# Optimization experiments

Hardware: AMD Instinct MI355X
Metric: run time of the kernel (lower is better)

## Reference

```python
import jax, jax.numpy as jnp
import numpy as np

B, C, K = 8192, 4096, 4096
BK, BN = 1, 16          # block-sparse tile sizes (bk x bn)
KEEP = 0.3


def setup_inputs() -> dict:
    key = jax.random.key(0)
    kx, kw, kb, km = jax.random.split(key, 4)
    stdv = 1.0 / np.sqrt(C * K)  # reset_parameters uses 1/sqrt(C*K)
    x = jax.random.normal(kx, (B, C), dtype=jnp.float32)
    weight = jax.random.uniform(kw, (K, C), dtype=jnp.float32, minval=-stdv, maxval=stdv)
    # block mask on (K/bk, C/bn) grid, expanded to full weight shape
    blk = (jax.random.uniform(km, (K // BK, C // BN)) < KEEP).astype(jnp.float32)
    mask = jnp.repeat(jnp.repeat(blk, BK, axis=0), BN, axis=1)  # [K, C]
    weight = weight * mask
    bias = jax.random.uniform(kb, (K,), dtype=jnp.float32, minval=-stdv, maxval=stdv)
    return {"x": x, "weight": weight, "bias": bias}


def reference(x, weight, bias):
    # SparseLinearRelu forward (sparse-kernel path, attr='relu'):
    # y = relu(x @ W^T + b); zero blocks of W contribute nothing (skipped by kernel).
    return jax.nn.relu(jnp.dot(x, weight.T) + bias)
```

## Files before the change

kernel.cpp:

```cpp
#include <hip/hip_runtime.h>
#include <hip/hip_bf16.h>

typedef __attribute__((ext_vector_type(4))) float f32x4;
typedef __attribute__((ext_vector_type(8))) short bf16x8;
typedef __attribute__((ext_vector_type(4))) short bf16x4v;

#define M_DIM 8192
#define N_DIM 4096
#define K_DIM 4096
#define NX (M_DIM * K_DIM)
#define NW (N_DIM * K_DIM)

#define BM 256
#define BN 256
#define BK 64
#define NKT (K_DIM / BK)
#define THREADS 512

#define GLOAD_LDS16(g, l)                                                        \
  __builtin_amdgcn_global_load_lds(                                              \
      (const __attribute__((address_space(1))) void*)(g),                        \
      (__attribute__((address_space(3))) void*)(l), 16, 0, 0)

__global__ __launch_bounds__(256) void convert_bf16(const float* __restrict__ x,
                                                    const float* __restrict__ w,
                                                    short* __restrict__ ws) {
  const long stride = (long)gridDim.x * blockDim.x;
  const long total8 = ((long)NX + NW) / 8;
  for (long i = blockIdx.x * (long)blockDim.x + threadIdx.x; i < total8; i += stride) {
    const long base = i * 8;
    const float* src = (base < NX) ? (x + base) : (w + (base - NX));
    short* dst = ws + base;
    f32x4 a = *(const f32x4*)src;
    f32x4 b = *(const f32x4*)(src + 4);
    bf16x8 o;
    o[0] = (short)__bfloat16_as_ushort(__float2bfloat16(a[0]));
    o[1] = (short)__bfloat16_as_ushort(__float2bfloat16(a[1]));
    o[2] = (short)__bfloat16_as_ushort(__float2bfloat16(a[2]));
    o[3] = (short)__bfloat16_as_ushort(__float2bfloat16(a[3]));
    o[4] = (short)__bfloat16_as_ushort(__float2bfloat16(b[0]));
    o[5] = (short)__bfloat16_as_ushort(__float2bfloat16(b[1]));
    o[6] = (short)__bfloat16_as_ushort(__float2bfloat16(b[2]));
    o[7] = (short)__bfloat16_as_ushort(__float2bfloat16(b[3]));
    *(bf16x8*)dst = o;
  }
}

__global__ __launch_bounds__(THREADS, 2) void gemm256_bf16(
    const short* __restrict__ Abf,
    const short* __restrict__ Bbf,
    const float* __restrict__ bias,
    float* __restrict__ Y) {
  __shared__ short lds[2 * 32768];
  char* const ldsb = (char*)lds;

  const int tid  = threadIdx.x;
  const int lane = tid & 63;
  const int wave = tid >> 6;
  const int wm   = wave >> 2;
  const int wn   = wave & 3;

  const int lin = blockIdx.x + blockIdx.y * (N_DIM / BN);
  const int swz = (lin & 7) * 64 + (lin >> 3);
  const int bx = swz & 15;
  const int by = swz >> 4;
  const long rowA0 = (long)by * BM;
  const long rowB0 = (long)bx * BN;

  const int sg_col = (((lane & 7) ^ ((lane >> 3) & 7)) << 3);
  const int s_row  = wave * 8 + (lane >> 3);
  const int voff = s_row * K_DIM + sg_col;

  const short* uA = Abf + rowA0 * (long)K_DIM;
  const short* uB = Bbf + rowB0 * (long)K_DIM;

  const int offk0 = (lane & 15) * 128 + ((((lane >> 4)) ^ (lane & 7)) << 4);
  const int offk1 = (lane & 15) * 128 + (((4 + (lane >> 4)) ^ (lane & 7)) << 4);

#define STAGE_HALF(BOFF_, HALF_, TT) do {                                        \
    const short* u_ = ((HALF_) < 2 ? uA : uB) +                                  \
                      (long)(((HALF_) & 1) * 128) * K_DIM + (long)(TT) * BK;     \
    char* l_ = ldsb + (BOFF_) + ((HALF_) < 2 ? 0 : 32768) +                      \
               ((HALF_) & 1) * 16384 + wave * 1024;                              \
    GLOAD_LDS16(u_ + voff, l_);                                                  \
    GLOAD_LDS16(u_ + 64 * K_DIM + voff, l_ + 8192);                              \
  } while (0)

#define PH_READ_A(DST, BOFF_, MADD) do {                                         \
    const char* pa_ = ldsb + (BOFF_) + wm * 16384 + (MADD);                      \
    _Pragma("unroll")                                                            \
    for (int m_ = 0; m_ < 4; ++m_) {                                             \
      DST[m_][0] = *(const bf16x8*)(pa_ + m_ * 2048 + offk0);                    \
      DST[m_][1] = *(const bf16x8*)(pa_ + m_ * 2048 + offk1);                    \
    }                                                                            \
  } while (0)

#define PH_READ_B(DST, BOFF_, NADD) do {                                         \
    const char* pb_ = ldsb + (BOFF_) + 32768 + wn * 8192 + (NADD);               \
    _Pragma("unroll")                                                            \
    for (int n_ = 0; n_ < 2; ++n_) {                                             \
      DST[n_][0] = *(const bf16x8*)(pb_ + n_ * 2048 + offk0);                    \
      DST[n_][1] = *(const bf16x8*)(pb_ + n_ * 2048 + offk1);                    \
    }                                                                            \
  } while (0)

#define MFMA16(AF, BF, MB, NB) do {                                              \
    __builtin_amdgcn_s_setprio(1);                                               \
    _Pragma("unroll")                                                            \
    for (int kk_ = 0; kk_ < 2; ++kk_)                                            \
      _Pragma("unroll")                                                          \
      for (int m_ = 0; m_ < 4; ++m_)                                             \
        _Pragma("unroll")                                                        \
        for (int n_ = 0; n_ < 2; ++n_)                                           \
          acc[(MB) + m_][(NB) + n_] = __builtin_amdgcn_mfma_f32_16x16x32_bf16(   \
              AF[m_][kk_], BF[n_][kk_], acc[(MB) + m_][(NB) + n_], 0, 0, 0);     \
    __builtin_amdgcn_s_setprio(0);                                               \
  } while (0)

#define TILE(BOFF_, NOFF_, T, DO_ST, BCUR, BNXT, RDNXT, VM) do {                 \
                                                                        \
    PH_READ_A(af, BOFF_, 0);                                                     \
    MFMA16(af, BCUR, 0, 0);                                                      \
                                                                        \
    PH_READ_B(b23, BOFF_, 4096);                                                 \
    MFMA16(af, b23, 0, 2);                                                       \
    __builtin_amdgcn_s_barrier();                                                \
                                                                        \
    if (DO_ST) { STAGE_HALF(BOFF_, 2, (T) + 2); STAGE_HALF(BOFF_, 3, (T) + 2); } \
    PH_READ_A(af, BOFF_, 8192);                                                  \
    MFMA16(af, BCUR, 4, 0);                                                      \
    __builtin_amdgcn_s_barrier();                                                \
                                                                        \
    if ((VM) == 4)      asm volatile("s_waitcnt vmcnt(4)" ::: "memory");         \
    else if ((VM) == 0) asm volatile("s_waitcnt vmcnt(0)" ::: "memory");         \
    if ((VM) >= 0) __builtin_amdgcn_s_barrier();                \
    if (DO_ST) { STAGE_HALF(BOFF_, 0, (T) + 2); STAGE_HALF(BOFF_, 1, (T) + 2); } \
    if (RDNXT) PH_READ_B(BNXT, NOFF_, 0);                                        \
    MFMA16(af, b23, 4, 2);                                                       \
  } while (0)

  f32x4 acc[8][4];
#pragma unroll
  for (int i = 0; i < 8; ++i)
#pragma unroll
    for (int j = 0; j < 4; ++j) acc[i][j] = (f32x4)0.0f;

  bf16x8 af[4][2], b01X[2][2], b01Y[2][2], b23[2][2];

  STAGE_HALF(0, 0, 0);
  STAGE_HALF(0, 1, 0);
  STAGE_HALF(0, 2, 0);
  STAGE_HALF(0, 3, 0);
  STAGE_HALF(65536, 2, 1);
  STAGE_HALF(65536, 3, 1);
  STAGE_HALF(65536, 0, 1);
  STAGE_HALF(65536, 1, 1);
  asm volatile("s_waitcnt vmcnt(8)" ::: "memory");
  __builtin_amdgcn_s_barrier();
  PH_READ_B(b01X, 0, 0);

  for (int tp = 0; tp < NKT / 2 - 1; ++tp) {
    const int t0 = 2 * tp;
    TILE(0,     65536, t0,     1, b01X, b01Y, 1, 4);
    TILE(65536, 0,     t0 + 1, 1, b01Y, b01X, 1, 4);
  }
  TILE(0,     65536, NKT - 2, 0, b01X, b01Y, 1, 0);
  TILE(65536, 0,     NKT - 1, 0, b01Y, b01X, 0, -1);

#undef TILE
#undef MFMA16
#undef PH_READ_B
#undef PH_READ_A
#undef STAGE_HALF

  {
    char* scr = ldsb + wave * 8192;
    const int c0 = lane & 15;
    const int r0 = (lane >> 4) * 4;
    const int rd_row = lane >> 3;
    const int rd_ch  = (lane & 7) * 16;
#pragma unroll
    for (int jp = 0; jp < 2; ++jp) {
      const long gcb = rowB0 + wn * 64 + jp * 32 + (lane & 7) * 4;
      const f32x4 bv4 = *(const f32x4*)&bias[gcb];
#pragma unroll
      for (int i = 0; i < 8; ++i) {
#pragma unroll
        for (int r = 0; r < 4; ++r) {
          *(float*)(scr + (r0 + r) * 144 + c0 * 4)      = acc[i][2 * jp + 0][r];
          *(float*)(scr + (r0 + r) * 144 + 64 + c0 * 4) = acc[i][2 * jp + 1][r];
        }
        f32x4 v0 = *(const f32x4*)(scr + rd_row * 144 + rd_ch);
        f32x4 v1 = *(const f32x4*)(scr + (8 + rd_row) * 144 + rd_ch);
        v0 += bv4;
        v1 += bv4;
#pragma unroll
        for (int e = 0; e < 4; ++e) {
          v0[e] = fmaxf(v0[e], 0.0f);
          v1[e] = fmaxf(v1[e], 0.0f);
        }
        const long gr = rowA0 + wm * 128 + i * 16;
        *(f32x4*)&Y[(gr + rd_row) * (long)N_DIM + gcb]     = v0;
        *(f32x4*)&Y[(gr + 8 + rd_row) * (long)N_DIM + gcb] = v1;
      }
    }
  }
}

#define FBM 128
#define FBK 32
#define FLDSS 40
__global__ __launch_bounds__(256) void fallback_gemm(
    const float* __restrict__ X, const float* __restrict__ W,
    const float* __restrict__ bias, float* __restrict__ Y) {
  __shared__ short As[FBM * FLDSS];
  __shared__ short Bs[FBM * FLDSS];
  const int tid = threadIdx.x, lane = tid & 63, wave = tid >> 6;
  const int wm = (wave >> 1) * 64, wn = (wave & 1) * 64;
  const long rowA0 = (long)blockIdx.y * FBM, rowB0 = (long)blockIdx.x * FBM;
  const int srow = tid >> 3, scol = (tid & 7) * 4;
  const float* Aptr = X + (rowA0 + srow) * (long)K_DIM + scol;
  const float* Bptr = W + (rowB0 + srow) * (long)K_DIM + scol;
  f32x4 ra[4], rb[4];
#pragma unroll
  for (int i = 0; i < 4; ++i) {
    ra[i] = *(const f32x4*)(Aptr + (long)i * 32 * K_DIM);
    rb[i] = *(const f32x4*)(Bptr + (long)i * 32 * K_DIM);
  }
  f32x4 acc[4][4];
#pragma unroll
  for (int i = 0; i < 4; ++i)
#pragma unroll
    for (int j = 0; j < 4; ++j) acc[i][j] = (f32x4)0.0f;
  for (int kt = 0; kt < K_DIM / FBK; ++kt) {
    __syncthreads();
#pragma unroll
    for (int i = 0; i < 4; ++i) {
      bf16x4v pa, pb;
#pragma unroll
      for (int j = 0; j < 4; ++j) {
        pa[j] = (short)__bfloat16_as_ushort(__float2bfloat16(ra[i][j]));
        pb[j] = (short)__bfloat16_as_ushort(__float2bfloat16(rb[i][j]));
      }
      *(bf16x4v*)&As[(i * 32 + srow) * FLDSS + scol] = pa;
      *(bf16x4v*)&Bs[(i * 32 + srow) * FLDSS + scol] = pb;
    }
    if (kt + 1 < K_DIM / FBK) {
      const float* An = Aptr + (kt + 1) * FBK;
      const float* Bn = Bptr + (kt + 1) * FBK;
#pragma unroll
      for (int i = 0; i < 4; ++i) {
        ra[i] = *(const f32x4*)(An + (long)i * 32 * K_DIM);
        rb[i] = *(const f32x4*)(Bn + (long)i * 32 * K_DIM);
      }
    }
    __syncthreads();
    bf16x8 af[4], bfr[4];
#pragma unroll
    for (int i = 0; i < 4; ++i) {
      af[i]  = *(const bf16x8*)&As[(wm + i * 16 + (lane & 15)) * FLDSS + (lane >> 4) * 8];
      bfr[i] = *(const bf16x8*)&Bs[(wn + i * 16 + (lane & 15)) * FLDSS + (lane >> 4) * 8];
    }
#pragma unroll
    for (int i = 0; i < 4; ++i)
#pragma unroll
      for (int j = 0; j < 4; ++j)
        acc[i][j] = __builtin_amdgcn_mfma_f32_16x16x32_bf16(af[i], bfr[j], acc[i][j], 0, 0, 0);
  }
  const int r0 = (lane >> 4) * 4, c0 = lane & 15;
#pragma unroll
  for (int j = 0; j < 4; ++j) {
    const long gc = rowB0 + wn + j * 16 + c0;
    const float bv = bias[gc];
#pragma unroll
    for (int i = 0; i < 4; ++i) {
      const long gr0 = rowA0 + wm + i * 16 + r0;
#pragma unroll
      for (int r = 0; r < 4; ++r) {
        float v = acc[i][j][r] + bv;
        Y[(gr0 + r) * (long)N_DIM + gc] = fmaxf(v, 0.0f);
      }
    }
  }
}

extern "C" void kernel_launch(void* const* d_in, const int* in_sizes, int n_in,
                              void* d_out, int out_size, void* d_ws, size_t ws_size,
                              hipStream_t stream) {
  const float* x = (const float*)d_in[0];
  const float* w = (const float*)d_in[1];
  const float* b = (const float*)d_in[2];
  float* y = (float*)d_out;

  const size_t need = (size_t)(NX + NW) * sizeof(short);
  if (ws_size >= need) {
    short* ws = (short*)d_ws;
    convert_bf16<<<2048, 256, 0, stream>>>(x, w, ws);
    dim3 grid(N_DIM / BN, M_DIM / BM);
    gemm256_bf16<<<grid, dim3(THREADS), 0, stream>>>(ws, ws + NX, b, y);
  } else {
    dim3 grid(N_DIM / FBM, M_DIM / FBM);
    fallback_gemm<<<grid, dim3(256), 0, stream>>>(x, w, b, y);
  }
}
```

Before: 252.6 us.

## Interleave A/B quarter-tile loads with MFMA phases using per-phase barriers

Reorganizes the LDS layout so A and B tiles are split into interleaved row-halves and quarters, and restructures the main loop to issue one global-to-LDS staging chunk at the start of each of the four MFMA phases, each followed by a barrier and lgkmcnt wait. The intent is to spread global memory traffic evenly across the compute phases, in the style of a ping-pong schedule, instead of bursting two halves at a time. The vmcnt wait threshold is adjusted to match the new load ordering. The extra barriers per tile add synchronization overhead and could stall waves if the loads do not overlap well.

```diff
diff --git a/kernel.cpp b/kernel.cpp
--- a/kernel.cpp
+++ b/kernel.cpp
@@ -69,7 +69,9 @@
 
   const int sg_col = (((lane & 7) ^ ((lane >> 3) & 7)) << 3);
   const int s_row  = wave * 8 + (lane >> 3);
-  const int voff = s_row * K_DIM + sg_col;
+  const int voffA  = s_row * K_DIM + sg_col;
+  const int rowBl  = (s_row >> 5) * 64 + (s_row & 31);
+  const int voffB  = rowBl * K_DIM + sg_col;
 
   const short* uA = Abf + rowA0 * (long)K_DIM;
   const short* uB = Bbf + rowB0 * (long)K_DIM;
@@ -77,17 +79,22 @@
   const int offk0 = (lane & 15) * 128 + ((((lane >> 4)) ^ (lane & 7)) << 4);
   const int offk1 = (lane & 15) * 128 + (((4 + (lane >> 4)) ^ (lane & 7)) << 4);
 
-#define STAGE_HALF(BOFF_, HALF_, TT) do {                                        \
-    const short* u_ = ((HALF_) < 2 ? uA : uB) +                                  \
-                      (long)(((HALF_) & 1) * 128) * K_DIM + (long)(TT) * BK;     \
-    char* l_ = ldsb + (BOFF_) + ((HALF_) < 2 ? 0 : 32768) +                      \
-               ((HALF_) & 1) * 16384 + wave * 1024;                              \
-    GLOAD_LDS16(u_ + voff, l_);                                                  \
-    GLOAD_LDS16(u_ + 64 * K_DIM + voff, l_ + 8192);                              \
-  } while (0)
-
-#define PH_READ_A(DST, BOFF_, MADD) do {                                         \
-    const char* pa_ = ldsb + (BOFF_) + wm * 16384 + (MADD);                      \
+#define STAGE_AH(BOFF_, HALF_, TT) do {                                          \
+    const short* g_ = uA + (long)((HALF_) * 64) * K_DIM + (long)(TT) * BK + voffA;\
+    char* l_ = ldsb + (BOFF_) + (HALF_) * 16384 + wave * 1024;                   \
+    GLOAD_LDS16(g_, l_);                                                         \
+    GLOAD_LDS16(g_ + 128 * (long)K_DIM, l_ + 8192);                              \
+  } while (0)
+
+#define STAGE_BH(BOFF_, Q_, TT) do {                                             \
+    const short* g_ = uB + (long)((Q_) * 32) * K_DIM + (long)(TT) * BK + voffB;  \
+    char* l_ = ldsb + (BOFF_) + 32768 + (Q_) * 16384 + wave * 1024;              \
+    GLOAD_LDS16(g_, l_);                                                         \
+    GLOAD_LDS16(g_ + 128 * (long)K_DIM, l_ + 8192);                              \
+  } while (0)
+
+#define PH_READ_A(DST, BOFF_, HB) do {                                           \
+    const char* pa_ = ldsb + (BOFF_) + (HB) + wm * 8192;                         \
     _Pragma("unroll")                                                            \
     for (int m_ = 0; m_ < 4; ++m_) {                                             \
       DST[m_][0] = *(const bf16x8*)(pa_ + m_ * 2048 + offk0);                    \
@@ -95,8 +102,8 @@
     }                                                                            \
   } while (0)
 
-#define PH_READ_B(DST, BOFF_, NADD) do {                                         \
-    const char* pb_ = ldsb + (BOFF_) + 32768 + wn * 8192 + (NADD);               \
+#define PH_READ_B(DST, BOFF_, QB) do {                                           \
+    const char* pb_ = ldsb + (BOFF_) + 32768 + (QB) + wn * 4096;                 \
     _Pragma("unroll")                                                            \
     for (int n_ = 0; n_ < 2; ++n_) {                                             \
       DST[n_][0] = *(const bf16x8*)(pb_ + n_ * 2048 + offk0);                    \
@@ -117,26 +124,36 @@
     __builtin_amdgcn_s_setprio(0);                                               \
   } while (0)
 
+#define LGKM0 asm volatile("s_waitcnt lgkmcnt(0)" ::: "memory")
+#define BAR   __builtin_amdgcn_s_barrier()
+
 #define TILE(BOFF_, NOFF_, T, DO_ST, BCUR, BNXT, RDNXT, VM) do {                 \
-                                                                        \
+                        \
+    if (DO_ST) STAGE_BH(BOFF_, 0, (T) + 2);                                      \
     PH_READ_A(af, BOFF_, 0);                                                     \
+    BAR; LGKM0;                                                                  \
     MFMA16(af, BCUR, 0, 0);                                                      \
-                                                                        \
-    PH_READ_B(b23, BOFF_, 4096);                                                 \
+    BAR;                                                                         \
+                        \
+    if (DO_ST) STAGE_AH(BOFF_, 0, (T) + 2);                                      \
+    PH_READ_B(b23, BOFF_, 16384);                                                \
+    BAR; LGKM0;                                                                  \
     MFMA16(af, b23, 0, 2);                                                       \
-    __builtin_amdgcn_s_barrier();                                                \
-                                                                        \
-    if (DO_ST) { STAGE_HALF(BOFF_, 2, (T) + 2); STAGE_HALF(BOFF_, 3, (T) + 2); } \
-    PH_READ_A(af, BOFF_, 8192);                                                  \
+    BAR;                                                                         \
+                        \
+    if (DO_ST) STAGE_BH(BOFF_, 1, (T) + 2);                                      \
+    PH_READ_A(af, BOFF_, 16384);                                                 \
+    BAR; LGKM0;                                                                  \
     MFMA16(af, BCUR, 4, 0);                                                      \
-    __builtin_amdgcn_s_barrier();                                                \
-                                                                        \
-    if ((VM) == 4)      asm volatile("s_waitcnt vmcnt(4)" ::: "memory");         \
+    BAR;                                                                         \
+             \
+    if (DO_ST) STAGE_AH(BOFF_, 1, (T) + 2);                                      \
+    if ((VM) == 8)      asm volatile("s_waitcnt vmcnt(8)" ::: "memory");         \
     else if ((VM) == 0) asm volatile("s_waitcnt vmcnt(0)" ::: "memory");         \
-    if ((VM) >= 0) __builtin_amdgcn_s_barrier();                \
-    if (DO_ST) { STAGE_HALF(BOFF_, 0, (T) + 2); STAGE_HALF(BOFF_, 1, (T) + 2); } \
+    if ((VM) >= 0) BAR;                                    \
     if (RDNXT) PH_READ_B(BNXT, NOFF_, 0);                                        \
     MFMA16(af, b23, 4, 2);                                                       \
+    if ((VM) >= 0) BAR;                                   \
   } while (0)
 
   f32x4 acc[8][4];
@@ -147,31 +164,34 @@
 
   bf16x8 af[4][2], b01X[2][2], b01Y[2][2], b23[2][2];
 
-  STAGE_HALF(0, 0, 0);
-  STAGE_HALF(0, 1, 0);
-  STAGE_HALF(0, 2, 0);
-  STAGE_HALF(0, 3, 0);
-  STAGE_HALF(65536, 2, 1);
-  STAGE_HALF(65536, 3, 1);
-  STAGE_HALF(65536, 0, 1);
-  STAGE_HALF(65536, 1, 1);
+  STAGE_BH(0, 0, 0);
+  STAGE_AH(0, 0, 0);
+  STAGE_BH(0, 1, 0);
+  STAGE_AH(0, 1, 0);
+  STAGE_BH(65536, 0, 1);
+  STAGE_AH(65536, 0, 1);
+  STAGE_BH(65536, 1, 1);
+  STAGE_AH(65536, 1, 1);
   asm volatile("s_waitcnt vmcnt(8)" ::: "memory");
-  __builtin_amdgcn_s_barrier();
+  BAR;
   PH_READ_B(b01X, 0, 0);
 
   for (int tp = 0; tp < NKT / 2 - 1; ++tp) {
     const int t0 = 2 * tp;
-    TILE(0,     65536, t0,     1, b01X, b01Y, 1, 4);
-    TILE(65536, 0,     t0 + 1, 1, b01Y, b01X, 1, 4);
+    TILE(0,     65536, t0,     1, b01X, b01Y, 1, 8);
+    TILE(65536, 0,     t0 + 1, 1, b01Y, b01X, 1, 8);
   }
   TILE(0,     65536, NKT - 2, 0, b01X, b01Y, 1, 0);
   TILE(65536, 0,     NKT - 1, 0, b01Y, b01X, 0, -1);
 
 #undef TILE
+#undef LGKM0
+#undef BAR
 #undef MFMA16
 #undef PH_READ_B
 #undef PH_READ_A
-#undef STAGE_HALF
+#undef STAGE_BH
+#undef STAGE_AH
 
   {
     char* scr = ldsb + wave * 8192;
```

Measured after the change: 254.4 us. About the same (+0.7%).
